# Kernel tuning notes

Measured on AMD Instinct MI355X. Metric: run time of the kernel, lower is better.

## Reference

```python
import jax, jax.numpy as jnp
import numpy as np

B, D = 64, 65536   # batch, num default boxes
NEG_POS = 3        # negative:positive mining ratio (init arg)


def _bce_with_logits(x, t):
    # numerically stable elementwise BCE-with-logits (matches torch)
    return jnp.maximum(x, 0.0) - x * t + jnp.log1p(jnp.exp(-jnp.abs(x)))


def _smooth_l1(d):
    ad = jnp.abs(d)
    return jnp.where(ad < 1.0, 0.5 * d * d, ad - 0.5)


def setup_inputs() -> dict:
    key = jax.random.key(0)
    k1, k2, k3, k4 = jax.random.split(key, 4)
    loc_data = jax.random.normal(k1, (B, D, 4), dtype=jnp.float32)
    conf_data = jax.random.normal(k2, (B, D, 1), dtype=jnp.float32)
    loc_t = jax.random.normal(k3, (B, D, 4), dtype=jnp.float32)
    conf_t = (jax.random.uniform(k4, (B, D)) < 0.02).astype(jnp.int32)
    return {"loc_data": loc_data, "conf_data": conf_data,
            "loc_t": loc_t, "conf_t": conf_t}


def reference(loc_data, conf_data, loc_t, conf_t):
    pos = conf_t > 0                                  # [B, D]
    num_pos = pos.sum(axis=1, keepdims=True)          # [B, 1]

    # ---- localization loss: smooth-L1 mean over positive box coords ----
    pf = pos[:, :, None].astype(loc_data.dtype)       # [B, D, 1]
    sl1 = _smooth_l1(loc_data - loc_t) * pf           # [B, D, 4]
    n_loc_elems = pf.sum() * 4.0                      # masked-gather -> mean
    loss_l = sl1.sum() / n_loc_elems

    # ---- confidence loss with hard negative mining ----
    logits = conf_data[:, :, 0]                       # [B, D]
    bce = _bce_with_logits(logits, conf_t.astype(logits.dtype))
    bce_neg = jnp.where(pos, 0.0, bce)                # zero-out positives
    # double argsort -> per-row rank of each element's loss (descending)
    loss_idx = jnp.argsort(-bce_neg, axis=1)          # [B, D]
    idx_rank = jnp.argsort(loss_idx, axis=1)          # [B, D]
    num_neg = jnp.minimum(num_pos * NEG_POS, D)       # [B, 1]
    neg = idx_rank < num_neg                          # top-k hardest negatives
    sel = (pos | neg).astype(logits.dtype)            # [B, D]
    loss_c = (bce * sel).sum() / sel.sum()            # mean over selected

    N = num_pos.sum().astype(logits.dtype)
    return (loss_l / N, loss_c / N)
```

## Files before the change

kernel.cpp:

```cpp
#include <hip/hip_runtime.h>
#include <stdint.h>


#define B_ 64
#define D_ 65536
#define NEGPOS 3
#define BPR 16
#define NBLK (B_ * BPR)
#define CHUNK (D_ / BPR)
#define XC 1.25f
#define HBINS 4096
#define XRANGE 5.0f
#define CJCAP 1024

#define OFF_SL1P   0
#define OFF_BCEP   8192
#define OFF_NP     16384
#define OFF_CC     20480
#define OFF_NEGSUM 24576
#define OFF_KSEL   25088
#define OFF_CAND   32768

__device__ __forceinline__ float softplus_f(float x) {
    return fmaxf(x, 0.0f) + log1pf(expf(-fabsf(x)));
}

__device__ __forceinline__ int bin_of_x(float x) {
    int b = (int)((x - XC) * ((float)HBINS / XRANGE));
    return max(0, min(HBINS - 1, b));
}

__device__ __forceinline__ float smooth_l1_4(float4 a, float4 b) {
    float s = 0.0f, d, ad;
    d = a.x - b.x; ad = fabsf(d); s += (ad < 1.0f) ? 0.5f * d * d : ad - 0.5f;
    d = a.y - b.y; ad = fabsf(d); s += (ad < 1.0f) ? 0.5f * d * d : ad - 0.5f;
    d = a.z - b.z; ad = fabsf(d); s += (ad < 1.0f) ? 0.5f * d * d : ad - 0.5f;
    d = a.w - b.w; ad = fabsf(d); s += (ad < 1.0f) ? 0.5f * d * d : ad - 0.5f;
    return s;
}

__device__ __forceinline__ double wredD(double v) {
#pragma unroll
    for (int o = 32; o > 0; o >>= 1) v += __shfl_down(v, o, 64);
    return v;
}
__device__ __forceinline__ int wredI(int v) {
#pragma unroll
    for (int o = 32; o > 0; o >>= 1) v += __shfl_down(v, o, 64);
    return v;
}

__device__ __forceinline__ int blockSumI(int v, int* sh) {
    int w = wredI(v);
    const int lane = threadIdx.x & 63, wid = threadIdx.x >> 6;
    __syncthreads();
    if (lane == 0) sh[wid] = w;
    __syncthreads();
    return sh[0] + sh[1] + sh[2] + sh[3];
}

__global__ void __launch_bounds__(256)
mbl_k1(const float4* __restrict__ loc4, const float* __restrict__ conf,
       const float4* __restrict__ loct4, const int* __restrict__ conft,
       unsigned char* __restrict__ ws)
{
    __shared__ float lcand[CHUNK];
    __shared__ unsigned short lpos[CHUNK];
    __shared__ unsigned wtot[4];
    __shared__ double wrD[8];

    const int block = blockIdx.x;
    const int base = block * CHUNK;
    const int lane = threadIdx.x & 63, wid = threadIdx.x >> 6;

    const float4* c4 = (const float4*)(conf + base);
    const int4*   t4 = (const int4*)(conft + base);

    float4 xv[4]; int4 tv[4];
#pragma unroll
    for (int it = 0; it < 4; it++) {
        const int g = threadIdx.x + it * 256;
        xv[it] = c4[g];
        tv[it] = t4[g];
    }

    double bcp = 0.0;
    unsigned cntc = 0, cntp = 0;
#pragma unroll
    for (int it = 0; it < 4; it++) {
#pragma unroll
        for (int c = 0; c < 4; c++) {
            float x = (c == 0) ? xv[it].x : (c == 1) ? xv[it].y : (c == 2) ? xv[it].z : xv[it].w;
            int   t = (c == 0) ? tv[it].x : (c == 1) ? tv[it].y : (c == 2) ? tv[it].z : tv[it].w;
            if (t > 0) { cntp++; bcp += (double)(softplus_f(x) - x); }
            else if (x >= XC) cntc++;
        }
    }

    unsigned pk = (cntc << 16) | cntp;
    unsigned incl = pk;
#pragma unroll
    for (int o = 1; o < 64; o <<= 1) {
        unsigned v = __shfl_up(incl, o, 64);
        if (lane >= o) incl += v;
    }
    unsigned excl = incl - pk;
    if (lane == 63) wtot[wid] = incl;
    __syncthreads();
    unsigned wbase = 0;
    for (int w = 0; w < wid; w++) wbase += wtot[w];
    const unsigned tot = wtot[0] + wtot[1] + wtot[2] + wtot[3];
    const unsigned totc = tot >> 16, totp = tot & 0xFFFFu;
    unsigned offc = (excl >> 16) + (wbase >> 16);
    unsigned offp = (excl & 0xFFFFu) + (wbase & 0xFFFFu);

#pragma unroll
    for (int it = 0; it < 4; it++) {
#pragma unroll
        for (int c = 0; c < 4; c++) {
            float x = (c == 0) ? xv[it].x : (c == 1) ? xv[it].y : (c == 2) ? xv[it].z : xv[it].w;
            int   t = (c == 0) ? tv[it].x : (c == 1) ? tv[it].y : (c == 2) ? tv[it].z : tv[it].w;
            const int li = (threadIdx.x + it * 256) * 4 + c;
            if (t > 0) lpos[offp++] = (unsigned short)li;
            else if (x >= XC) lcand[offc++] = x;
        }
    }
    __syncthreads();

    float* seg = (float*)(ws + OFF_CAND) + (size_t)block * CHUNK;
    for (unsigned i = threadIdx.x; i < totc; i += 256) seg[i] = lcand[i];

    double sl1 = 0.0;
    for (unsigned i = threadIdx.x; i < totp; i += 256) {
        const int e = base + (int)lpos[i];
        sl1 += (double)smooth_l1_4(loc4[e], loct4[e]);
    }

    double s1 = wredD(sl1), s2 = wredD(bcp);
    if (lane == 0) { wrD[wid] = s1; wrD[4 + wid] = s2; }
    __syncthreads();
    if (threadIdx.x == 0) {
        ((double*)(ws + OFF_SL1P))[block] = wrD[0] + wrD[1] + wrD[2] + wrD[3];
        ((double*)(ws + OFF_BCEP))[block] = wrD[4] + wrD[5] + wrD[6] + wrD[7];
        ((unsigned*)(ws + OFF_NP))[block] = totp;
        ((unsigned*)(ws + OFF_CC))[block] = totc;
    }
}

__global__ void __launch_bounds__(256)
mbl_k2(const float* __restrict__ conf, const int* __restrict__ conft,
       unsigned char* __restrict__ ws)
{
    __shared__ unsigned hist[HBINS];
    __shared__ float ubuf[CJCAP];
    __shared__ unsigned wsuf[4], sccS[BPR];
    __shared__ double wrD[4];
    __shared__ int shI[4];
    __shared__ unsigned shJ, shRemJ, shNP, shT, shCj;

    const int row = blockIdx.x;
    const int lane = threadIdx.x & 63, wid = threadIdx.x >> 6;

    if (wid == 0) {
        const unsigned* ccp = (const unsigned*)(ws + OFF_CC) + row * BPR;
        const unsigned* npp = (const unsigned*)(ws + OFF_NP) + row * BPR;
        unsigned c = (lane < BPR) ? ccp[lane] : 0u;
        unsigned p = (lane < BPR) ? npp[lane] : 0u;
        if (lane < BPR) sccS[lane] = c;
        unsigned ct = c, pt = p;
#pragma unroll
        for (int o = 1; o < BPR; o <<= 1) {
            ct += __shfl_down(ct, o, 64);
            pt += __shfl_down(pt, o, 64);
        }
        if (lane == 0) { shT = ct; shNP = pt; shCj = 0; }
    }
    __syncthreads();

    const int np = (int)shNP;
    const unsigned n = shT;
    long long k = (long long)np * NEGPOS;
    if (k > D_) k = D_;
    long long negs = (long long)D_ - np;
    if (k > negs) k = negs;
    if (threadIdx.x == 0) ((int*)(ws + OFF_KSEL))[row] = (int)k;

    bool done = false, fb = false;
    if (k <= 0) {
        if (threadIdx.x == 0) ((double*)(ws + OFF_NEGSUM))[row] = 0.0;
        done = true;
    } else if ((long long)n < k) {
        fb = true;
    }

    if (!done && !fb) {
        const int s = threadIdx.x >> 4, li = threadIdx.x & 15;
        const unsigned cs = sccS[s];
        const float4* seg4 = (const float4*)((const float*)(ws + OFF_CAND)
                             + (size_t)(row * BPR + s) * CHUNK);

        for (int i = threadIdx.x; i < HBINS; i += 256) hist[i] = 0;
        __syncthreads();

        for (unsigned i0 = (unsigned)li * 4u; i0 < cs; i0 += 64u) {
            const float4 q = seg4[i0 >> 2];
            if (i0 + 0 < cs) atomicAdd(&hist[bin_of_x(q.x)], 1u);
            if (i0 + 1 < cs) atomicAdd(&hist[bin_of_x(q.y)], 1u);
            if (i0 + 2 < cs) atomicAdd(&hist[bin_of_x(q.z)], 1u);
            if (i0 + 3 < cs) atomicAdd(&hist[bin_of_x(q.w)], 1u);
        }
        __syncthreads();

        unsigned s16 = 0;
        const int b0i = threadIdx.x * 16;
#pragma unroll
        for (int j = 0; j < 16; j++) s16 += hist[b0i + j];
        unsigned suf = s16;
#pragma unroll
        for (int o = 1; o < 64; o <<= 1) {
            unsigned v = __shfl_down(suf, o, 64);
            if (lane + o < 64) suf += v;
        }
        if (lane == 0) wsuf[wid] = suf;
        __syncthreads();
        unsigned addw = 0;
        for (int w = wid + 1; w < 4; w++) addw += wsuf[w];
        suf += addw;
        const unsigned sufx = suf - s16;
        if ((long long)sufx < k && (long long)suf >= k) {
            long long cum = sufx;
            for (int j = 15; j >= 0; j--) {
                cum += hist[b0i + j];
                if (cum >= k) {
                    shJ = (unsigned)(b0i + j);
                    shRemJ = (unsigned)(k - (cum - (long long)hist[b0i + j]));
                    break;
                }
            }
        }
        __syncthreads();
        const unsigned J = shJ, remJ = shRemJ;

        double acc = 0.0;
        for (unsigned i0 = (unsigned)li * 4u; i0 < cs; i0 += 64u) {
            const float4 q = seg4[i0 >> 2];
#pragma unroll
            for (int c = 0; c < 4; c++) {
                if (i0 + (unsigned)c < cs) {
                    const float x = (c == 0) ? q.x : (c == 1) ? q.y : (c == 2) ? q.z : q.w;
                    const int b = bin_of_x(x);
                    if (b > (int)J) acc += (double)softplus_f(x);
                    else if (b == (int)J) {
                        unsigned sl = atomicAdd(&shCj, 1u);
                        if (sl < CJCAP) ubuf[sl] = x;
                    }
                }
            }
        }
        __syncthreads();
        const unsigned cj = shCj;

        if (cj <= CJCAP) {
            for (unsigned i = threadIdx.x; i < cj; i += 256) {
                const float xi = ubuf[i];
                unsigned r = 0;
                for (unsigned l = 0; l < cj; l++) {
                    const float xl = ubuf[l];
                    r += (xl > xi || (xl == xi && l < i)) ? 1u : 0u;
                }
                if (r < remJ) acc += (double)softplus_f(xi);
            }
            double t = wredD(acc);
            if (lane == 0) wrD[wid] = t;
            __syncthreads();
            if (threadIdx.x == 0)
                ((double*)(ws + OFF_NEGSUM))[row] =
                    wrD[0] + wrD[1] + wrD[2] + wrD[3];
            done = true;
        } else fb = true;
    }

    if (!done && fb) {
        const float* rowc = conf + row * D_;
        const int*   rowt = conft + row * D_;
        unsigned lo = 0u, hi = 0xFFFFFFFFu;
        for (int it = 0; it < 32; it++) {
            const unsigned mid = lo + ((hi - lo) >> 1);
            unsigned um = (mid & 0x80000000u) ? (mid & 0x7FFFFFFFu) : ~mid;
            float fm = __uint_as_float(um);
            int c = 0;
            for (int i = threadIdx.x; i < D_; i += 256)
                if (rowt[i] <= 0 && rowc[i] > fm) c++;
            const int tot = blockSumI(c, shI);
            if ((long long)tot >= k) lo = mid; else hi = mid;
        }
        unsigned uT = (hi & 0x80000000u) ? (hi & 0x7FFFFFFFu) : ~hi;
        float xT = __uint_as_float(uT);
        int c = 0;
        double acc = 0.0;
        for (int i = threadIdx.x; i < D_; i += 256) {
            if (rowt[i] <= 0) {
                float x = rowc[i];
                if (x > xT) { c++; acc += (double)softplus_f(x); }
            }
        }
        int rem = (int)(k - (long long)blockSumI(c, shI));
        double t = wredD(acc);
        if (lane == 0) wrD[wid] = t;
        __syncthreads();
        if (threadIdx.x == 0)
            ((double*)(ws + OFF_NEGSUM))[row] =
                wrD[0] + wrD[1] + wrD[2] + wrD[3] +
                (double)rem * (double)softplus_f(xT);
    }
}

__global__ void __launch_bounds__(256)
mbl_k5(unsigned char* __restrict__ ws, float* __restrict__ out)
{
    __shared__ double wrA[4], wrB[4], wrC[4];
    __shared__ int shN[4], shK[4];
    const double* sl1p = (const double*)(ws + OFF_SL1P);
    const double* bcep = (const double*)(ws + OFF_BCEP);
    const unsigned* npb = (const unsigned*)(ws + OFF_NP);
    const int* ksel = (const int*)(ws + OFF_KSEL);
    const double* ns = (const double*)(ws + OFF_NEGSUM);

    double a = 0.0, b = 0.0, c = 0.0;
    int n = 0, kk = 0;
    for (int i = threadIdx.x; i < NBLK; i += 256) {
        a += sl1p[i]; b += bcep[i]; n += (int)npb[i];
    }
    if (threadIdx.x < B_) { kk = ksel[threadIdx.x]; c = ns[threadIdx.x]; }

    double ra = wredD(a), rb = wredD(b), rc = wredD(c);
    int rn = wredI(n), rk = wredI(kk);
    const int lane = threadIdx.x & 63, wid = threadIdx.x >> 6;
    if (lane == 0) { wrA[wid] = ra; wrB[wid] = rb; wrC[wid] = rc; shN[wid] = rn; shK[wid] = rk; }
    __syncthreads();
    if (threadIdx.x == 0) {
        double SL1 = wrA[0] + wrA[1] + wrA[2] + wrA[3];
        double BCE = wrB[0] + wrB[1] + wrB[2] + wrB[3];
        double NSUM = wrC[0] + wrC[1] + wrC[2] + wrC[3];
        double Np = (double)(shN[0] + shN[1] + shN[2] + shN[3]);
        double Kt = (double)(shK[0] + shK[1] + shK[2] + shK[3]);
        double out0 = (Np > 0.0) ? (SL1 / (4.0 * Np)) / Np : 0.0;
        double denom = Np + Kt;
        double out1 = (Np > 0.0 && denom > 0.0) ? ((BCE + NSUM) / denom) / Np : 0.0;
        out[0] = (float)out0;
        out[1] = (float)out1;
    }
}

extern "C" void kernel_launch(void* const* d_in, const int* in_sizes, int n_in,
                              void* d_out, int out_size, void* d_ws, size_t ws_size,
                              hipStream_t stream)
{
    const float4* loc4  = (const float4*)d_in[0];
    const float*  conf  = (const float*)d_in[1];
    const float4* loct4 = (const float4*)d_in[2];
    const int*    conft = (const int*)d_in[3];
    unsigned char* ws = (unsigned char*)d_ws;
    float* out = (float*)d_out;

    mbl_k1<<<dim3(NBLK), dim3(256), 0, stream>>>(loc4, conf, loct4, conft, ws);
    mbl_k2<<<dim3(B_), dim3(256), 0, stream>>>(conf, conft, ws);
    mbl_k5<<<dim3(1), dim3(256), 0, stream>>>(ws, out);
}
```

Measured before the change: 174.7 us.

## Build per-block histograms and fixed-point bin sums in k1, reduce in k2

Result: faster. 168.1 us (-3.7%).

```diff
diff --git a/kernel.cpp b/kernel.cpp
--- a/kernel.cpp
+++ b/kernel.cpp
@@ -9,9 +9,14 @@
 #define NBLK (B_ * BPR)
 #define CHUNK (D_ / BPR)
 #define XC 1.25f
-#define HBINS 4096
+#define HB512 512
 #define XRANGE 5.0f
 #define CJCAP 1024
+
+#define FXS 274877906944.0
+#define FXI (1.0 / 274877906944.0)
+
+typedef unsigned long long ull;
 
 #define OFF_SL1P   0
 #define OFF_BCEP   8192
@@ -19,15 +24,17 @@
 #define OFF_CC     20480
 #define OFF_NEGSUM 24576
 #define OFF_KSEL   25088
-#define OFF_CAND   32768
+#define OFF_HIST   32768
+#define OFF_BSUM   2129920
+#define OFF_CAND   8388608
 
 __device__ __forceinline__ float softplus_f(float x) {
     return fmaxf(x, 0.0f) + log1pf(expf(-fabsf(x)));
 }
 
 __device__ __forceinline__ int bin_of_x(float x) {
-    int b = (int)((x - XC) * ((float)HBINS / XRANGE));
-    return max(0, min(HBINS - 1, b));
+    int b = (int)((x - XC) * ((float)HB512 / XRANGE));
+    return max(0, min(HB512 - 1, b));
 }
 
 __device__ __forceinline__ float smooth_l1_4(float4 a, float4 b) {
@@ -49,6 +56,11 @@
     for (int o = 32; o > 0; o >>= 1) v += __shfl_down(v, o, 64);
     return v;
 }
+__device__ __forceinline__ ull wredU64(ull v) {
+#pragma unroll
+    for (int o = 32; o > 0; o >>= 1) v += __shfl_down(v, o, 64);
+    return v;
+}
 
 __device__ __forceinline__ int blockSumI(int v, int* sh) {
     int w = wredI(v);
@@ -66,12 +78,18 @@
 {
     __shared__ float lcand[CHUNK];
     __shared__ unsigned short lpos[CHUNK];
+    __shared__ unsigned lhist[HB512];
+    __shared__ ull lbsum[HB512];
     __shared__ unsigned wtot[4];
     __shared__ double wrD[8];
 
     const int block = blockIdx.x;
     const int base = block * CHUNK;
-    const int lane = threadIdx.x & 63, wid = threadIdx.x >> 6;
+    const int tid = threadIdx.x;
+    const int lane = tid & 63, wid = tid >> 6;
+
+    lhist[tid] = 0u;       lhist[tid + 256] = 0u;
+    lbsum[tid] = 0ull;     lbsum[tid + 256] = 0ull;
 
     const float4* c4 = (const float4*)(conf + base);
     const int4*   t4 = (const int4*)(conft + base);
@@ -79,7 +97,7 @@
     float4 xv[4]; int4 tv[4];
 #pragma unroll
     for (int it = 0; it < 4; it++) {
-        const int g = threadIdx.x + it * 256;
+        const int g = tid + it * 256;
         xv[it] = c4[g];
         tv[it] = t4[g];
     }
@@ -120,7 +138,7 @@
         for (int c = 0; c < 4; c++) {
             float x = (c == 0) ? xv[it].x : (c == 1) ? xv[it].y : (c == 2) ? xv[it].z : xv[it].w;
             int   t = (c == 0) ? tv[it].x : (c == 1) ? tv[it].y : (c == 2) ? tv[it].z : tv[it].w;
-            const int li = (threadIdx.x + it * 256) * 4 + c;
+            const int li = (tid + it * 256) * 4 + c;
             if (t > 0) lpos[offp++] = (unsigned short)li;
             else if (x >= XC) lcand[offc++] = x;
         }
@@ -128,10 +146,17 @@
     __syncthreads();
 
     float* seg = (float*)(ws + OFF_CAND) + (size_t)block * CHUNK;
-    for (unsigned i = threadIdx.x; i < totc; i += 256) seg[i] = lcand[i];
+    for (unsigned i = tid; i < totc; i += 256) seg[i] = lcand[i];
+
+    for (unsigned i = tid; i < totc; i += 256) {
+        const float x = lcand[i];
+        const int b = bin_of_x(x);
+        atomicAdd(&lhist[b], 1u);
+        atomicAdd(&lbsum[b], (ull)((double)softplus_f(x) * FXS + 0.5));
+    }
 
     double sl1 = 0.0;
-    for (unsigned i = threadIdx.x; i < totp; i += 256) {
+    for (unsigned i = tid; i < totp; i += 256) {
         const int e = base + (int)lpos[i];
         sl1 += (double)smooth_l1_4(loc4[e], loct4[e]);
     }
@@ -139,7 +164,17 @@
     double s1 = wredD(sl1), s2 = wredD(bcp);
     if (lane == 0) { wrD[wid] = s1; wrD[4 + wid] = s2; }
     __syncthreads();
-    if (threadIdx.x == 0) {
+
+    {
+        unsigned* gh = (unsigned*)(ws + OFF_HIST) + (size_t)block * HB512;
+        ull*      gb = (ull*)(ws + OFF_BSUM) + (size_t)block * HB512;
+        gh[tid]       = lhist[tid];
+        gh[tid + 256] = lhist[tid + 256];
+        gb[tid]       = lbsum[tid];
+        gb[tid + 256] = lbsum[tid + 256];
+    }
+
+    if (tid == 0) {
         ((double*)(ws + OFF_SL1P))[block] = wrD[0] + wrD[1] + wrD[2] + wrD[3];
         ((double*)(ws + OFF_BCEP))[block] = wrD[4] + wrD[5] + wrD[6] + wrD[7];
         ((unsigned*)(ws + OFF_NP))[block] = totp;
@@ -151,15 +186,16 @@
 mbl_k2(const float* __restrict__ conf, const int* __restrict__ conft,
        unsigned char* __restrict__ ws)
 {
-    __shared__ unsigned hist[HBINS];
     __shared__ float ubuf[CJCAP];
     __shared__ unsigned wsuf[4], sccS[BPR];
     __shared__ double wrD[4];
+    __shared__ ull wrU[4];
     __shared__ int shI[4];
-    __shared__ unsigned shJ, shRemJ, shNP, shT, shCj;
+    __shared__ unsigned shJ, shRemJ, shNP, shT, shCj, shCJN;
 
     const int row = blockIdx.x;
-    const int lane = threadIdx.x & 63, wid = threadIdx.x >> 6;
+    const int tid = threadIdx.x;
+    const int lane = tid & 63, wid = tid >> 6;
 
     if (wid == 0) {
         const unsigned* ccp = (const unsigned*)(ws + OFF_CC) + row * BPR;
@@ -183,39 +219,30 @@
     if (k > D_) k = D_;
     long long negs = (long long)D_ - np;
     if (k > negs) k = negs;
-    if (threadIdx.x == 0) ((int*)(ws + OFF_KSEL))[row] = (int)k;
+    if (tid == 0) ((int*)(ws + OFF_KSEL))[row] = (int)k;
 
     bool done = false, fb = false;
     if (k <= 0) {
-        if (threadIdx.x == 0) ((double*)(ws + OFF_NEGSUM))[row] = 0.0;
+        if (tid == 0) ((double*)(ws + OFF_NEGSUM))[row] = 0.0;
         done = true;
     } else if ((long long)n < k) {
         fb = true;
     }
 
     if (!done && !fb) {
-        const int s = threadIdx.x >> 4, li = threadIdx.x & 15;
-        const unsigned cs = sccS[s];
-        const float4* seg4 = (const float4*)((const float*)(ws + OFF_CAND)
-                             + (size_t)(row * BPR + s) * CHUNK);
-
-        for (int i = threadIdx.x; i < HBINS; i += 256) hist[i] = 0;
-        __syncthreads();
-
-        for (unsigned i0 = (unsigned)li * 4u; i0 < cs; i0 += 64u) {
-            const float4 q = seg4[i0 >> 2];
-            if (i0 + 0 < cs) atomicAdd(&hist[bin_of_x(q.x)], 1u);
-            if (i0 + 1 < cs) atomicAdd(&hist[bin_of_x(q.y)], 1u);
-            if (i0 + 2 < cs) atomicAdd(&hist[bin_of_x(q.z)], 1u);
-            if (i0 + 3 < cs) atomicAdd(&hist[bin_of_x(q.w)], 1u);
-        }
-        __syncthreads();
-
-        unsigned s16 = 0;
-        const int b0i = threadIdx.x * 16;
-#pragma unroll
-        for (int j = 0; j < 16; j++) s16 += hist[b0i + j];
-        unsigned suf = s16;
+        const unsigned* ghrow = (const unsigned*)(ws + OFF_HIST) + (size_t)row * BPR * HB512;
+        const ull*      gbrow = (const ull*)(ws + OFF_BSUM) + (size_t)row * BPR * HB512;
+        unsigned rc0 = 0, rc1 = 0;
+        ull bs0 = 0, bs1 = 0;
+        for (int s = 0; s < BPR; s++) {
+            const uint2 h2 = ((const uint2*)(ghrow + s * HB512))[tid];
+            rc0 += h2.x; rc1 += h2.y;
+            bs0 += gbrow[s * HB512 + 2 * tid];
+            bs1 += gbrow[s * HB512 + 2 * tid + 1];
+        }
+
+        const unsigned s2 = rc0 + rc1;
+        unsigned suf = s2;
 #pragma unroll
         for (int o = 1; o < 64; o <<= 1) {
             unsigned v = __shfl_down(suf, o, 64);
@@ -226,42 +253,46 @@
         unsigned addw = 0;
         for (int w = wid + 1; w < 4; w++) addw += wsuf[w];
         suf += addw;
-        const unsigned sufx = suf - s16;
+        const unsigned sufx = suf - s2;
         if ((long long)sufx < k && (long long)suf >= k) {
-            long long cum = sufx;
-            for (int j = 15; j >= 0; j--) {
-                cum += hist[b0i + j];
-                if (cum >= k) {
-                    shJ = (unsigned)(b0i + j);
-                    shRemJ = (unsigned)(k - (cum - (long long)hist[b0i + j]));
-                    break;
-                }
-            }
+            const long long cum = (long long)sufx + rc1;
+            if (cum >= k) { shJ = 2 * tid + 1; shRemJ = (unsigned)(k - sufx); shCJN = rc1; }
+            else          { shJ = 2 * tid;     shRemJ = (unsigned)(k - cum);  shCJN = rc0; }
         }
         __syncthreads();
-        const unsigned J = shJ, remJ = shRemJ;
-
-        double acc = 0.0;
-        for (unsigned i0 = (unsigned)li * 4u; i0 < cs; i0 += 64u) {
-            const float4 q = seg4[i0 >> 2];
-#pragma unroll
-            for (int c = 0; c < 4; c++) {
-                if (i0 + (unsigned)c < cs) {
-                    const float x = (c == 0) ? q.x : (c == 1) ? q.y : (c == 2) ? q.z : q.w;
-                    const int b = bin_of_x(x);
-                    if (b > (int)J) acc += (double)softplus_f(x);
-                    else if (b == (int)J) {
-                        unsigned sl = atomicAdd(&shCj, 1u);
-                        if (sl < CJCAP) ubuf[sl] = x;
+        const unsigned J = shJ, remJ = shRemJ, cjn = shCJN;
+
+        if (cjn > CJCAP) {
+            fb = true;
+        } else {
+            ull part = 0;
+            if (2 * tid > (int)J) part += bs0;
+            if (2 * tid + 1 > (int)J) part += bs1;
+            ull pw = wredU64(part);
+            if (lane == 0) wrU[wid] = pw;
+
+            const int s = tid >> 4, li = tid & 15;
+            const unsigned cs = sccS[s];
+            const float4* seg4 = (const float4*)((const float*)(ws + OFF_CAND)
+                                 + (size_t)(row * BPR + s) * CHUNK);
+            for (unsigned i0 = (unsigned)li * 4u; i0 < cs; i0 += 64u) {
+                const float4 q = seg4[i0 >> 2];
+#pragma unroll
+                for (int c = 0; c < 4; c++) {
+                    if (i0 + (unsigned)c < cs) {
+                        const float x = (c == 0) ? q.x : (c == 1) ? q.y : (c == 2) ? q.z : q.w;
+                        if ((unsigned)bin_of_x(x) == J) {
+                            unsigned sl = atomicAdd(&shCj, 1u);
+                            if (sl < CJCAP) ubuf[sl] = x;
+                        }
                     }
                 }
             }
-        }
-        __syncthreads();
-        const unsigned cj = shCj;
-
-        if (cj <= CJCAP) {
-            for (unsigned i = threadIdx.x; i < cj; i += 256) {
+            __syncthreads();
+            const unsigned cj = shCj;
+
+            double acc = 0.0;
+            for (unsigned i = tid; i < cj; i += 256) {
                 const float xi = ubuf[i];
                 unsigned r = 0;
                 for (unsigned l = 0; l < cj; l++) {
@@ -270,14 +301,16 @@
                 }
                 if (r < remJ) acc += (double)softplus_f(xi);
             }
-            double t = wredD(acc);
-            if (lane == 0) wrD[wid] = t;
+            double t2 = wredD(acc);
+            if (lane == 0) wrD[wid] = t2;
             __syncthreads();
-            if (threadIdx.x == 0)
-                ((double*)(ws + OFF_NEGSUM))[row] =
-                    wrD[0] + wrD[1] + wrD[2] + wrD[3];
+            if (tid == 0) {
+                const ull NU = wrU[0] + wrU[1] + wrU[2] + wrU[3];
+                const double CJ = wrD[0] + wrD[1] + wrD[2] + wrD[3];
+                ((double*)(ws + OFF_NEGSUM))[row] = (double)NU * FXI + CJ;
+            }
             done = true;
-        } else fb = true;
+        }
     }
 
     if (!done && fb) {
@@ -289,7 +322,7 @@
             unsigned um = (mid & 0x80000000u) ? (mid & 0x7FFFFFFFu) : ~mid;
             float fm = __uint_as_float(um);
             int c = 0;
-            for (int i = threadIdx.x; i < D_; i += 256)
+            for (int i = tid; i < D_; i += 256)
                 if (rowt[i] <= 0 && rowc[i] > fm) c++;
             const int tot = blockSumI(c, shI);
             if ((long long)tot >= k) lo = mid; else hi = mid;
@@ -298,17 +331,17 @@
         float xT = __uint_as_float(uT);
         int c = 0;
         double acc = 0.0;
-        for (int i = threadIdx.x; i < D_; i += 256) {
+        for (int i = tid; i < D_; i += 256) {
             if (rowt[i] <= 0) {
                 float x = rowc[i];
                 if (x > xT) { c++; acc += (double)softplus_f(x); }
             }
         }
         int rem = (int)(k - (long long)blockSumI(c, shI));
-        double t = wredD(acc);
-        if (lane == 0) wrD[wid] = t;
+        double t2 = wredD(acc);
+        if (lane == 0) wrD[wid] = t2;
         __syncthreads();
-        if (threadIdx.x == 0)
+        if (tid == 0)
             ((double*)(ws + OFF_NEGSUM))[row] =
                 wrD[0] + wrD[1] + wrD[2] + wrD[3] +
                 (double)rem * (double)softplus_f(xT);
```
